# Optimization experiments

Measured on AMD Instinct MI355X. Metric: run time of the kernel, lower is better.

## Reference

```python
import jax, jax.numpy as jnp
import numpy as np

N_NODES = 50000
N_EDGES = 800000


def gcn_layer(x, edge_index, W, b):
    # GCNConv with normalize=False: out[i] = sum_{(j->i) in E} (x_j @ W) + b
    src, dst = edge_index[0], edge_index[1]
    h = x @ W                          # [N, F_out] transform first (cheaper)
    msg = h[src]                       # [E, F_out] gather
    agg = jax.ops.segment_sum(msg, dst, num_segments=x.shape[0])  # scatter-sum
    return agg + b


def setup_inputs() -> dict:
    key = jax.random.key(0)
    ks = jax.random.split(key, 6)
    x = jax.random.normal(ks[0], (N_NODES, 128), dtype=jnp.float32)
    edge_index = jax.random.randint(ks[1], (2, N_EDGES), 0, N_NODES, dtype=jnp.int64)
    # Glorot-ish scaling for stability through 3 layers
    W1 = jax.random.normal(ks[2], (128, 256), dtype=jnp.float32) * (1.0 / np.sqrt(128))
    W2 = jax.random.normal(ks[3], (256, 256), dtype=jnp.float32) * (1.0 / np.sqrt(256))
    W3 = jax.random.normal(ks[4], (256, 256), dtype=jnp.float32) * (1.0 / np.sqrt(256))
    b1 = jnp.zeros((256,), jnp.float32)
    b2 = jnp.zeros((256,), jnp.float32)
    b3 = jnp.zeros((256,), jnp.float32)
    return {"x": x, "edge_index": edge_index, "W1": W1, "b1": b1,
            "W2": W2, "b2": b2, "W3": W3, "b3": b3}


def reference(x, edge_index, W1, b1, W2, b2, W3, b3):
    h = jax.nn.relu(gcn_layer(x, edge_index, W1, b1))
    h = jax.nn.relu(gcn_layer(h, edge_index, W2, b2))
    h = jax.nn.relu(gcn_layer(h, edge_index, W3, b3))
    return h
```

## Files before the change

### kernel.cpp

```cpp
#include <hip/hip_runtime.h>
#include <hip/hip_bf16.h>


#define NBIN 98
#define BINSH 9
#define CAP 10240

typedef short bf16x8 __attribute__((ext_vector_type(8)));
typedef float f32x4 __attribute__((ext_vector_type(4)));

__device__ __forceinline__ short f2bf(float f) {
    __hip_bfloat16 b = __float2bfloat16(f);
    return *reinterpret_cast<short*>(&b);
}
__device__ __forceinline__ float bf2f(short s) {
    union { unsigned u; float f; } c;
    c.u = ((unsigned)(unsigned short)s) << 16;
    return c.f;
}

__device__ __forceinline__ void acc8(float* a, uint4 v) {
    unsigned w[4] = { v.x, v.y, v.z, v.w };
#pragma unroll
    for (int i = 0; i < 4; ++i) {
        union { unsigned u; float f; } lo, hi;
        lo.u = w[i] << 16;
        hi.u = w[i] & 0xFFFF0000u;
        a[2 * i]     += lo.f;
        a[2 * i + 1] += hi.f;
    }
}

__global__ void prep(const float* __restrict__ W1, const float* __restrict__ W2,
                     const float* __restrict__ W3, const float4* __restrict__ x,
                     short* __restrict__ Wt1, short* __restrict__ Wt2,
                     short* __restrict__ Wt3, short* __restrict__ xb) {
    int idx = blockIdx.x * 256 + threadIdx.x;
    if (idx < 32768) {
        int n = idx >> 7, k = idx & 127;
        Wt1[idx] = f2bf(W1[k * 256 + n]);
    } else if (idx < 98304) {
        int i = idx - 32768, n = i >> 8, k = i & 255;
        Wt2[i] = f2bf(W2[k * 256 + n]);
    } else if (idx < 163840) {
        int i = idx - 98304, n = i >> 8, k = i & 255;
        Wt3[i] = f2bf(W3[k * 256 + n]);
    } else {
        int i = idx - 163840;
        if (i < 1600000) {
            float4 v = x[i];
            short tmp[4] = { f2bf(v.x), f2bf(v.y), f2bf(v.z), f2bf(v.w) };
            *reinterpret_cast<uint2*>(&xb[i * 4]) = *reinterpret_cast<uint2*>(tmp);
        }
    }
}


__global__ void bin_fill(const int* __restrict__ ei, int* __restrict__ gcursor,
                         unsigned* __restrict__ staging, int E) {
    __shared__ int h[NBIN];
    __shared__ int cur[NBIN];
    for (int i = threadIdx.x; i < NBIN; i += 256) h[i] = 0;
    __syncthreads();
    int base = blockIdx.x * 4096;
    int d_[16], s_[16];
#pragma unroll
    for (int i = 0; i < 16; ++i) {
        int e = base + i * 256 + threadIdx.x;
        if (e < E) {
            s_[i] = ei[e];
            d_[i] = ei[E + e];
            atomicAdd(&h[d_[i] >> BINSH], 1);
        } else d_[i] = -1;
    }
    __syncthreads();
    for (int i = threadIdx.x; i < NBIN; i += 256)
        cur[i] = h[i] ? atomicAdd(&gcursor[i], h[i]) : 0;
    __syncthreads();
#pragma unroll
    for (int i = 0; i < 16; ++i) {
        if (d_[i] >= 0) {
            int bin = d_[i] >> BINSH;
            int p = atomicAdd(&cur[bin], 1);
            staging[(size_t)bin * CAP + p] =
                ((unsigned)(d_[i] & 511) << 16) | (unsigned)s_[i];
        }
    }
}

__global__ void binbase_scan(const int* __restrict__ gcursor, int* __restrict__ binbase,
                             int* __restrict__ off, int E, int N) {
    __shared__ int lds[128];
    int t = threadIdx.x;
    int v = (t < NBIN) ? gcursor[t] : 0;
    lds[t] = v;
    __syncthreads();
    for (int d = 1; d < 128; d <<= 1) {
        int a = (t >= d) ? lds[t - d] : 0;
        __syncthreads();
        lds[t] += a;
        __syncthreads();
    }
    if (t < NBIN) binbase[t] = lds[t] - v;
    if (t == 0) off[N] = E;
}

__launch_bounds__(256)
__global__ void bin_finalize(const unsigned* __restrict__ staging,
                             const int* __restrict__ cnt, const int* __restrict__ binbase,
                             int* __restrict__ off, int* __restrict__ csr, int N) {
    __shared__ unsigned sorted[CAP];
    __shared__ int sb[128];
    __shared__ int nd_c[512];
    __shared__ int nd_pos[512];
    __shared__ int psum[256];
    const int b = blockIdx.x, t = threadIdx.x;
    const int n = cnt[b];
    const unsigned* reg = staging + (size_t)b * CAP;
    const int gbase = binbase[b];

    if (t < 128) sb[t] = 0;
    nd_c[t] = 0; nd_c[t + 256] = 0;
    __syncthreads();
    for (int p = t; p < n; p += 256) {
        unsigned v = reg[p];
        atomicAdd(&sb[(v & 0xFFFFu) >> BINSH], 1);
        atomicAdd(&nd_c[v >> 16], 1);
    }
    __syncthreads();
    int myc = (t < 128) ? sb[t] : 0;
    for (int d = 1; d < 128; d <<= 1) {
        int a = (t < 128 && t >= d) ? sb[t - d] : 0;
        __syncthreads();
        if (t < 128) sb[t] += a;
        __syncthreads();
    }
    if (t < 128) sb[t] -= myc;
    int c0 = nd_c[2 * t], c1 = nd_c[2 * t + 1];
    psum[t] = c0 + c1;
    __syncthreads();
    for (int d = 1; d < 256; d <<= 1) {
        int a = (t >= d) ? psum[t - d] : 0;
        __syncthreads();
        psum[t] += a;
        __syncthreads();
    }
    int ebase = gbase + (t ? psum[t - 1] : 0);
    int nb0 = b << BINSH;
    nd_pos[2 * t]     = ebase;
    nd_pos[2 * t + 1] = ebase + c0;
    if (nb0 + 2 * t < N)     off[nb0 + 2 * t]     = ebase;
    if (nb0 + 2 * t + 1 < N) off[nb0 + 2 * t + 1] = ebase + c0;
    __syncthreads();
    for (int p = t; p < n; p += 256) {
        unsigned v = reg[p];
        int pos = atomicAdd(&sb[(v & 0xFFFFu) >> BINSH], 1);
        sorted[pos] = v;
    }
    __syncthreads();
    for (int p = t; p < n; p += 256) {
        unsigned v = sorted[p];
        int pos = atomicAdd(&nd_pos[v >> 16], 1);
        csr[pos] = (int)(v & 0xFFFFu);
    }
}


__global__ void gather256(const short* __restrict__ h, short* __restrict__ agg,
                          const int* __restrict__ off, const int* __restrict__ csr,
                          int N) {
    const int gw = (blockIdx.x * blockDim.x + threadIdx.x) >> 6;
    if (gw >= N) return;
    const int lane = threadIdx.x & 63;
    const int half = lane >> 5, l = lane & 31;
    const int col = l * 8;
    const int base = off[gw];
    const int d = off[gw + 1] - base;

    float acc[8];
#pragma unroll
    for (int q = 0; q < 8; ++q) acc[q] = 0.0f;

    int j = 0;
    for (; j + 8 <= d; j += 8) {
        int s0 = csr[base + j + half];
        int s1 = csr[base + j + 2 + half];
        int s2 = csr[base + j + 4 + half];
        int s3 = csr[base + j + 6 + half];
        uint4 v0 = *reinterpret_cast<const uint4*>(h + (size_t)s0 * 256 + col);
        uint4 v1 = *reinterpret_cast<const uint4*>(h + (size_t)s1 * 256 + col);
        uint4 v2 = *reinterpret_cast<const uint4*>(h + (size_t)s2 * 256 + col);
        uint4 v3 = *reinterpret_cast<const uint4*>(h + (size_t)s3 * 256 + col);
        acc8(acc, v0); acc8(acc, v1); acc8(acc, v2); acc8(acc, v3);
    }
    for (; j + 2 <= d; j += 2) {
        int s = csr[base + j + half];
        uint4 v = *reinterpret_cast<const uint4*>(h + (size_t)s * 256 + col);
        acc8(acc, v);
    }
    if (j < d && half == 0) {
        int s = csr[base + j];
        uint4 v = *reinterpret_cast<const uint4*>(h + (size_t)s * 256 + col);
        acc8(acc, v);
    }
#pragma unroll
    for (int q = 0; q < 8; ++q) acc[q] += __shfl_xor(acc[q], 32);
    if (half == 0) {
        short o[8];
#pragma unroll
        for (int q = 0; q < 8; ++q) o[q] = f2bf(acc[q]);
        *reinterpret_cast<uint4*>(agg + (size_t)gw * 256 + col) =
            *reinterpret_cast<uint4*>(o);
    }
}

__global__ void gather128(const short* __restrict__ h, short* __restrict__ agg,
                          const int* __restrict__ off, const int* __restrict__ csr,
                          int N) {
    const int gw = (blockIdx.x * blockDim.x + threadIdx.x) >> 6;
    if (gw >= N) return;
    const int lane = threadIdx.x & 63;
    const int q4 = lane >> 4, l = lane & 15;
    const int col = l * 8;
    const int base = off[gw];
    const int d = off[gw + 1] - base;

    float acc[8];
#pragma unroll
    for (int q = 0; q < 8; ++q) acc[q] = 0.0f;

    int j = 0;
    for (; j + 8 <= d; j += 8) {
        int s0 = csr[base + j + q4];
        int s1 = csr[base + j + 4 + q4];
        uint4 v0 = *reinterpret_cast<const uint4*>(h + (size_t)s0 * 128 + col);
        uint4 v1 = *reinterpret_cast<const uint4*>(h + (size_t)s1 * 128 + col);
        acc8(acc, v0); acc8(acc, v1);
    }
    for (; j + 4 <= d; j += 4) {
        int s = csr[base + j + q4];
        uint4 v = *reinterpret_cast<const uint4*>(h + (size_t)s * 128 + col);
        acc8(acc, v);
    }
    int rem = d - j;
    if (q4 < rem) {
        int s = csr[base + j + q4];
        uint4 v = *reinterpret_cast<const uint4*>(h + (size_t)s * 128 + col);
        acc8(acc, v);
    }
#pragma unroll
    for (int q = 0; q < 8; ++q) {
        acc[q] += __shfl_xor(acc[q], 32);
        acc[q] += __shfl_xor(acc[q], 16);
    }
    if (q4 == 0) {
        short o[8];
#pragma unroll
        for (int q = 0; q < 8; ++q) o[q] = f2bf(acc[q]);
        *reinterpret_cast<uint4*>(agg + (size_t)gw * 128 + col) =
            *reinterpret_cast<uint4*>(o);
    }
}


template <typename OutT>
__launch_bounds__(512)
__global__ void gemm_bias_relu(const short* __restrict__ A, const short* __restrict__ Wt,
                               const float* __restrict__ bias, OutT* __restrict__ out,
                               int M, int K) {
    __shared__ short As[128][72];
    __shared__ short Bs[256][72];

    const int tid = threadIdx.x;
    const int lane = tid & 63, wid = tid >> 6;
    const int wr = wid >> 2, wc = wid & 3;
    const int lr = lane & 15, lg = lane >> 4;
    const int m0 = blockIdx.x * 128;

    f32x4 acc[4][4];
#pragma unroll
    for (int i = 0; i < 4; ++i)
#pragma unroll
        for (int j = 0; j < 4; ++j)
#pragma unroll
            for (int r = 0; r < 4; ++r) acc[i][j][r] = 0.0f;

    const int srA = tid >> 2;
    const int scA = (tid & 3) << 4;
    const int srB = tid >> 1;
    const int scB = (tid & 1) << 5;

    for (int k0 = 0; k0 < K; k0 += 64) {
        __syncthreads();
        {
            int gm = m0 + srA;
            if (gm < M) {
                const uint4* ap = reinterpret_cast<const uint4*>(A + (size_t)gm * K + k0 + scA);
                *reinterpret_cast<uint4*>(&As[srA][scA])     = ap[0];
                *reinterpret_cast<uint4*>(&As[srA][scA + 8]) = ap[1];
            } else {
                uint4 z = {0, 0, 0, 0};
                *reinterpret_cast<uint4*>(&As[srA][scA])     = z;
                *reinterpret_cast<uint4*>(&As[srA][scA + 8]) = z;
            }
            const uint4* bp = reinterpret_cast<const uint4*>(Wt + (size_t)srB * K + k0 + scB);
            *reinterpret_cast<uint4*>(&Bs[srB][scB])      = bp[0];
            *reinterpret_cast<uint4*>(&Bs[srB][scB + 8])  = bp[1];
            *reinterpret_cast<uint4*>(&Bs[srB][scB + 16]) = bp[2];
            *reinterpret_cast<uint4*>(&Bs[srB][scB + 24]) = bp[3];
        }
        __syncthreads();

#pragma unroll
        for (int ksub = 0; ksub < 2; ++ksub) {
            const int kb = ksub * 32 + 4 * lg;
            bf16x8 a[4], b[4];
#pragma unroll
            for (int mi = 0; mi < 4; ++mi) {
                int row = wr * 64 + mi * 16 + lr;
                uint2* pa = reinterpret_cast<uint2*>(&a[mi]);
                pa[0] = *reinterpret_cast<const uint2*>(&As[row][kb]);
                pa[1] = *reinterpret_cast<const uint2*>(&As[row][kb + 16]);
            }
#pragma unroll
            for (int ni = 0; ni < 4; ++ni) {
                int row = wc * 64 + ni * 16 + lr;
                uint2* pb = reinterpret_cast<uint2*>(&b[ni]);
                pb[0] = *reinterpret_cast<const uint2*>(&Bs[row][kb]);
                pb[1] = *reinterpret_cast<const uint2*>(&Bs[row][kb + 16]);
            }
#pragma unroll
            for (int mi = 0; mi < 4; ++mi)
#pragma unroll
                for (int ni = 0; ni < 4; ++ni)
                    acc[mi][ni] = __builtin_amdgcn_mfma_f32_16x16x32_bf16(a[mi], b[ni], acc[mi][ni], 0, 0, 0);
        }
    }

    float bv[4];
#pragma unroll
    for (int ni = 0; ni < 4; ++ni) bv[ni] = bias[wc * 64 + ni * 16 + lr];
#pragma unroll
    for (int mi = 0; mi < 4; ++mi) {
        int gmBase = m0 + wr * 64 + mi * 16 + 4 * lg;
#pragma unroll
        for (int r = 0; r < 4; ++r) {
            int gm = gmBase + r;
            if (gm >= M) continue;
#pragma unroll
            for (int ni = 0; ni < 4; ++ni) {
                int gn = wc * 64 + ni * 16 + lr;
                float v = acc[mi][ni][r] + bv[ni];
                v = v > 0.0f ? v : 0.0f;
                if constexpr (sizeof(OutT) == 2)
                    out[(size_t)gm * 256 + gn] = (OutT)f2bf(v);
                else
                    out[(size_t)gm * 256 + gn] = (OutT)v;
            }
        }
    }
}

extern "C" void kernel_launch(void* const* d_in, const int* in_sizes, int n_in,
                              void* d_out, int out_size, void* d_ws, size_t ws_size,
                              hipStream_t stream) {
    const float* x  = (const float*)d_in[0];
    const int*   ei = (const int*)d_in[1];
    const float* W1 = (const float*)d_in[2];
    const float* b1 = (const float*)d_in[3];
    const float* W2 = (const float*)d_in[4];
    const float* b2 = (const float*)d_in[5];
    const float* W3 = (const float*)d_in[6];
    const float* b3 = (const float*)d_in[7];
    float* out = (float*)d_out;
    short* hb  = (short*)d_out;

    const int Nn = 50000, E = 800000, F0 = 128, F = 256;
    const int EB = (E + 4095) / 4096;

    short* aggb = (short*)d_ws;
    short* xb   = aggb + (size_t)Nn * F;
    short* Wt1  = xb + (size_t)Nn * F0;
    short* Wt2  = Wt1 + F0 * F;
    short* Wt3  = Wt2 + F * F;
    int* off     = (int*)(Wt3 + F * F);
    int* gcursor = off + Nn + 1;
    int* binbase = gcursor + NBIN;
    unsigned* staging = (unsigned*)(binbase + NBIN);
    int* csr     = (int*)(staging + (size_t)NBIN * CAP);

    prep<<<(163840 + 1600000 + 255) / 256, 256, 0, stream>>>(
        W1, W2, W3, (const float4*)x, Wt1, Wt2, Wt3, xb);

    hipMemsetAsync(gcursor, 0, NBIN * 4, stream);
    bin_fill<<<EB, 256, 0, stream>>>(ei, gcursor, staging, E);
    binbase_scan<<<1, 128, 0, stream>>>(gcursor, binbase, off, E, Nn);
    bin_finalize<<<NBIN, 256, 0, stream>>>(staging, gcursor, binbase, off, csr, Nn);

    const int gemmGrid = (Nn + 127) / 128;
    const int gatherBlocks = (Nn * 64 + 255) / 256;

    gather128<<<gatherBlocks, 256, 0, stream>>>(xb, aggb, off, csr, Nn);
    gemm_bias_relu<short><<<gemmGrid, 512, 0, stream>>>(aggb, Wt1, b1, hb, Nn, F0);

    gather256<<<gatherBlocks, 256, 0, stream>>>(hb, aggb, off, csr, Nn);
    gemm_bias_relu<short><<<gemmGrid, 512, 0, stream>>>(aggb, Wt2, b2, hb, Nn, F);

    gather256<<<gatherBlocks, 256, 0, stream>>>(hb, aggb, off, csr, Nn);
    gemm_bias_relu<float><<<gemmGrid, 512, 0, stream>>>(aggb, Wt3, b3, out, Nn, F);
}
```

Measured before the change: 245.9 us.

## Merge CSR-build launches, drop source-sort pass, deepen gather unroll

Folds the gcursor memset and off[N] write into the prep kernel and replaces the separate binbase scan kernel with a per-block reduction over earlier bin counts inside bin_finalize. This removes two launches and a serial dependency from the CSR build. The finalize step no longer counting-sorts edges by source block before scattering, so each node's CSR order becomes arbitrary, which may hurt gather locality and makes float accumulation order nondeterministic. The gather loops now unroll to 16 edges per iteration so more loads are in flight, at the cost of extra registers.

```diff
diff --git a/kernel.cpp b/kernel.cpp
--- a/kernel.cpp
+++ b/kernel.cpp
@@ -12,11 +12,6 @@
 __device__ __forceinline__ short f2bf(float f) {
     __hip_bfloat16 b = __float2bfloat16(f);
     return *reinterpret_cast<short*>(&b);
-}
-__device__ __forceinline__ float bf2f(short s) {
-    union { unsigned u; float f; } c;
-    c.u = ((unsigned)(unsigned short)s) << 16;
-    return c.f;
 }
 
 __device__ __forceinline__ void acc8(float* a, uint4 v) {
@@ -34,7 +29,9 @@
 __global__ void prep(const float* __restrict__ W1, const float* __restrict__ W2,
                      const float* __restrict__ W3, const float4* __restrict__ x,
                      short* __restrict__ Wt1, short* __restrict__ Wt2,
-                     short* __restrict__ Wt3, short* __restrict__ xb) {
+                     short* __restrict__ Wt3, short* __restrict__ xb,
+                     int* __restrict__ gcursor, int* __restrict__ off,
+                     int E, int N) {
     int idx = blockIdx.x * 256 + threadIdx.x;
     if (idx < 32768) {
         int n = idx >> 7, k = idx & 127;
@@ -51,6 +48,10 @@
             float4 v = x[i];
             short tmp[4] = { f2bf(v.x), f2bf(v.y), f2bf(v.z), f2bf(v.w) };
             *reinterpret_cast<uint2*>(&xb[i * 4]) = *reinterpret_cast<uint2*>(tmp);
+        } else {
+            int z = i - 1600000;
+            if (z < NBIN) gcursor[z] = 0;
+            if (z == NBIN) off[N] = E;
         }
     }
 }
@@ -88,54 +89,29 @@
     }
 }
 
-__global__ void binbase_scan(const int* __restrict__ gcursor, int* __restrict__ binbase,
-                             int* __restrict__ off, int E, int N) {
-    __shared__ int lds[128];
-    int t = threadIdx.x;
-    int v = (t < NBIN) ? gcursor[t] : 0;
-    lds[t] = v;
-    __syncthreads();
-    for (int d = 1; d < 128; d <<= 1) {
-        int a = (t >= d) ? lds[t - d] : 0;
-        __syncthreads();
-        lds[t] += a;
-        __syncthreads();
-    }
-    if (t < NBIN) binbase[t] = lds[t] - v;
-    if (t == 0) off[N] = E;
-}
-
 __launch_bounds__(256)
 __global__ void bin_finalize(const unsigned* __restrict__ staging,
-                             const int* __restrict__ cnt, const int* __restrict__ binbase,
+                             const int* __restrict__ cnt,
                              int* __restrict__ off, int* __restrict__ csr, int N) {
-    __shared__ unsigned sorted[CAP];
-    __shared__ int sb[128];
+    __shared__ int red[256];
     __shared__ int nd_c[512];
     __shared__ int nd_pos[512];
     __shared__ int psum[256];
     const int b = blockIdx.x, t = threadIdx.x;
     const int n = cnt[b];
     const unsigned* reg = staging + (size_t)b * CAP;
-    const int gbase = binbase[b];
-
-    if (t < 128) sb[t] = 0;
+
+    red[t] = (t < b) ? cnt[t] : 0;
     nd_c[t] = 0; nd_c[t + 256] = 0;
     __syncthreads();
-    for (int p = t; p < n; p += 256) {
-        unsigned v = reg[p];
-        atomicAdd(&sb[(v & 0xFFFFu) >> BINSH], 1);
-        atomicAdd(&nd_c[v >> 16], 1);
-    }
-    __syncthreads();
-    int myc = (t < 128) ? sb[t] : 0;
-    for (int d = 1; d < 128; d <<= 1) {
-        int a = (t < 128 && t >= d) ? sb[t - d] : 0;
-        __syncthreads();
-        if (t < 128) sb[t] += a;
-        __syncthreads();
-    }
-    if (t < 128) sb[t] -= myc;
+    for (int d = 128; d > 0; d >>= 1) {
+        if (t < d) red[t] += red[t + d];
+        __syncthreads();
+    }
+    const int gbase = red[0];
+
+    for (int p = t; p < n; p += 256) atomicAdd(&nd_c[reg[p] >> 16], 1);
+    __syncthreads();
     int c0 = nd_c[2 * t], c1 = nd_c[2 * t + 1];
     psum[t] = c0 + c1;
     __syncthreads();
@@ -154,12 +130,6 @@
     __syncthreads();
     for (int p = t; p < n; p += 256) {
         unsigned v = reg[p];
-        int pos = atomicAdd(&sb[(v & 0xFFFFu) >> BINSH], 1);
-        sorted[pos] = v;
-    }
-    __syncthreads();
-    for (int p = t; p < n; p += 256) {
-        unsigned v = sorted[p];
         int pos = atomicAdd(&nd_pos[v >> 16], 1);
         csr[pos] = (int)(v & 0xFFFFu);
     }
@@ -182,16 +152,16 @@
     for (int q = 0; q < 8; ++q) acc[q] = 0.0f;
 
     int j = 0;
-    for (; j + 8 <= d; j += 8) {
-        int s0 = csr[base + j + half];
-        int s1 = csr[base + j + 2 + half];
-        int s2 = csr[base + j + 4 + half];
-        int s3 = csr[base + j + 6 + half];
-        uint4 v0 = *reinterpret_cast<const uint4*>(h + (size_t)s0 * 256 + col);
-        uint4 v1 = *reinterpret_cast<const uint4*>(h + (size_t)s1 * 256 + col);
-        uint4 v2 = *reinterpret_cast<const uint4*>(h + (size_t)s2 * 256 + col);
-        uint4 v3 = *reinterpret_cast<const uint4*>(h + (size_t)s3 * 256 + col);
-        acc8(acc, v0); acc8(acc, v1); acc8(acc, v2); acc8(acc, v3);
+    for (; j + 16 <= d; j += 16) {
+        int s[8];
+#pragma unroll
+        for (int u = 0; u < 8; ++u) s[u] = csr[base + j + 2 * u + half];
+        uint4 v[8];
+#pragma unroll
+        for (int u = 0; u < 8; ++u)
+            v[u] = *reinterpret_cast<const uint4*>(h + (size_t)s[u] * 256 + col);
+#pragma unroll
+        for (int u = 0; u < 8; ++u) acc8(acc, v[u]);
     }
     for (; j + 2 <= d; j += 2) {
         int s = csr[base + j + half];
@@ -230,12 +200,16 @@
     for (int q = 0; q < 8; ++q) acc[q] = 0.0f;
 
     int j = 0;
-    for (; j + 8 <= d; j += 8) {
-        int s0 = csr[base + j + q4];
-        int s1 = csr[base + j + 4 + q4];
-        uint4 v0 = *reinterpret_cast<const uint4*>(h + (size_t)s0 * 128 + col);
-        uint4 v1 = *reinterpret_cast<const uint4*>(h + (size_t)s1 * 128 + col);
-        acc8(acc, v0); acc8(acc, v1);
+    for (; j + 16 <= d; j += 16) {
+        int s[4];
+#pragma unroll
+        for (int u = 0; u < 4; ++u) s[u] = csr[base + j + 4 * u + q4];
+        uint4 v[4];
+#pragma unroll
+        for (int u = 0; u < 4; ++u)
+            v[u] = *reinterpret_cast<const uint4*>(h + (size_t)s[u] * 128 + col);
+#pragma unroll
+        for (int u = 0; u < 4; ++u) acc8(acc, v[u]);
     }
     for (; j + 4 <= d; j += 4) {
         int s = csr[base + j + q4];
@@ -385,17 +359,14 @@
     short* Wt3  = Wt2 + F * F;
     int* off     = (int*)(Wt3 + F * F);
     int* gcursor = off + Nn + 1;
-    int* binbase = gcursor + NBIN;
-    unsigned* staging = (unsigned*)(binbase + NBIN);
+    unsigned* staging = (unsigned*)(gcursor + NBIN);
     int* csr     = (int*)(staging + (size_t)NBIN * CAP);
 
-    prep<<<(163840 + 1600000 + 255) / 256, 256, 0, stream>>>(
-        W1, W2, W3, (const float4*)x, Wt1, Wt2, Wt3, xb);
-
-    hipMemsetAsync(gcursor, 0, NBIN * 4, stream);
+    prep<<<(163840 + 1600000 + NBIN + 1 + 255) / 256, 256, 0, stream>>>(
+        W1, W2, W3, (const float4*)x, Wt1, Wt2, Wt3, xb, gcursor, off, E, Nn);
+
     bin_fill<<<EB, 256, 0, stream>>>(ei, gcursor, staging, E);
-    binbase_scan<<<1, 128, 0, stream>>>(gcursor, binbase, off, E, Nn);
-    bin_finalize<<<NBIN, 256, 0, stream>>>(staging, gcursor, binbase, off, csr, Nn);
+    bin_finalize<<<NBIN, 256, 0, stream>>>(staging, gcursor, off, csr, Nn);
 
     const int gemmGrid = (Nn + 127) / 128;
     const int gatherBlocks = (Nn * 64 + 255) / 256;
```

Result: slower. 253.5 us (+3.1%).
